# Optimization experiments

Measured on AMD Instinct MI355X. Metric: run time of the kernel, lower is better.

The kernel has to match this reference:

```python
import jax, jax.numpy as jnp
import numpy as np

N_USER = 50000
N_ITEM = 50000
E = 500000
D = 256
H = 8
DK = D // H
EPS = 1e-5
SQRT_DK = float(np.sqrt(DK))


def _layernorm(x, g, b):
    m = jnp.mean(x, axis=-1, keepdims=True)
    v = jnp.var(x, axis=-1, keepdims=True)
    return (x - m) * jax.lax.rsqrt(v + EPS) * g + b


def _etype_aggregate(h_src, h_dst, src, dst, n_dst, Wk, bk, Wq, bq, Wv, bv, pri, att, msg):
    # per-ntype K/Q/V projections, then per-relation head-wise transforms
    k = (h_src @ Wk + bk).reshape(-1, H, DK)
    v = (h_src @ Wv + bv).reshape(-1, H, DK)
    q = (h_dst @ Wq + bq).reshape(-1, H, DK)
    k = jnp.einsum('nhi,hij->nhj', k, att)
    v = jnp.einsum('nhi,hij->nhj', v, msg)
    # v_dot_u score per edge per head: [E, H]
    score = jnp.einsum('ehd,ehd->eh', q[dst], k[src]) * pri / SQRT_DK
    # edge_softmax normalized per destination node (per head)
    smax = jax.ops.segment_max(score, dst, num_segments=n_dst)
    ex = jnp.exp(score - smax[dst])
    ssum = jax.ops.segment_sum(ex, dst, num_segments=n_dst)
    a = ex / ssum[dst]
    # u_mul_e + sum reduce (zero-in-degree dst nodes get zeros, like DGL sum)
    t = jax.ops.segment_sum(v[src] * a[:, :, None], dst, num_segments=n_dst)
    return t.reshape(n_dst, D)


def _dst_update(t, h, Wa, ba, skip, g, b):
    alpha = jax.nn.sigmoid(skip)
    out = (t @ Wa + ba) * alpha + h * (1.0 - alpha)
    return _layernorm(out, g, b)


def _forward(h_user, h_item, src_ui, dst_ui, src_iu, dst_iu, Wk_user, bk_user, Wq_user, bq_user, Wv_user, bv_user, Wa_user, ba_user, ln_g_user, ln_b_user, skip_user, Wk_item, bk_item, Wq_item, bq_item, Wv_item, bv_item, Wa_item, ba_item, ln_g_item, ln_b_item, skip_item, pri_ui, att_ui, msg_ui, pri_iu, att_iu, msg_iu):
    # (user, click, item): k/v from src ntype 'user', q from dst ntype 'item'
    t_item = _etype_aggregate(h_user, h_item, src_ui, dst_ui, N_ITEM, Wk_user, bk_user, Wq_item, bq_item, Wv_user, bv_user, pri_ui, att_ui, msg_ui)
    # (item, rev_click, user)
    t_user = _etype_aggregate(h_item, h_user, src_iu, dst_iu, N_USER, Wk_item, bk_item, Wq_user, bq_user, Wv_item, bv_item, pri_iu, att_iu, msg_iu)
    # each ntype is dst of exactly one etype -> cross_reducer 'mean' is identity
    new_user = _dst_update(t_user, h_user, Wa_user, ba_user, skip_user, ln_g_user, ln_b_user)
    new_item = _dst_update(t_item, h_item, Wa_item, ba_item, skip_item, ln_g_item, ln_b_item)
    return jnp.stack([new_user, new_item])  # [2, N, D]


def setup_inputs() -> dict:
    key = jax.random.key(0)
    ks = jax.random.split(key, 16)

    def xavier(k, shape):
        s = np.sqrt(2.0 / (shape[-2] + shape[-1]))
        return (jax.random.normal(k, shape, dtype=jnp.float32) * s).astype(jnp.float32)

    inp = {}
    inp['h_user'] = jax.random.normal(ks[0], (N_USER, D), dtype=jnp.float32)
    inp['h_item'] = jax.random.normal(ks[1], (N_ITEM, D), dtype=jnp.float32)
    inp['src_ui'] = jax.random.randint(ks[2], (E,), 0, N_USER, dtype=jnp.int32)
    inp['dst_ui'] = jax.random.randint(ks[3], (E,), 0, N_ITEM, dtype=jnp.int32)
    inp['src_iu'] = jax.random.randint(ks[4], (E,), 0, N_ITEM, dtype=jnp.int32)
    inp['dst_iu'] = jax.random.randint(ks[5], (E,), 0, N_USER, dtype=jnp.int32)
    i = 6
    for nt in ['user', 'item']:
        for nm in ['k', 'q', 'v', 'a']:
            inp[f'W{nm}_{nt}'] = xavier(jax.random.fold_in(ks[i], hash(nm) % 1000), (D, D))
            inp[f'b{nm}_{nt}'] = jnp.zeros((D,), jnp.float32)
        i += 1
        inp[f'ln_g_{nt}'] = jnp.ones((D,), jnp.float32)
        inp[f'ln_b_{nt}'] = jnp.zeros((D,), jnp.float32)
        inp[f'skip_{nt}'] = jnp.ones((1,), jnp.float32)
    for et in ['ui', 'iu']:
        inp[f'pri_{et}'] = jnp.ones((H,), jnp.float32)
        inp[f'att_{et}'] = xavier(ks[i], (H, DK, DK)); i += 1
        inp[f'msg_{et}'] = xavier(ks[i], (H, DK, DK)); i += 1
    return inp


def reference(h_user, h_item, src_ui, dst_ui, src_iu, dst_iu, Wk_user, bk_user, Wq_user, bq_user, Wv_user, bv_user, Wa_user, ba_user, ln_g_user, ln_b_user, skip_user, Wk_item, bk_item, Wq_item, bq_item, Wv_item, bv_item, Wa_item, ba_item, ln_g_item, ln_b_item, skip_item, pri_ui, att_ui, msg_ui, pri_iu, att_iu, msg_iu):
    return _forward(h_user, h_item, src_ui, dst_ui, src_iu, dst_iu, Wk_user, bk_user, Wq_user, bq_user, Wv_user, bv_user, Wa_user, ba_user, ln_g_user, ln_b_user, skip_user, Wk_item, bk_item, Wq_item, bq_item, Wv_item, bv_item, Wa_item, ba_item, ln_g_item, ln_b_item, skip_item, pri_ui, att_ui, msg_ui, pri_iu, att_iu, msg_iu)
```

## Files before the change

### kernel.cpp

```cpp
#include <hip/hip_runtime.h>

#define NN 50000
#define DD 256
#define HH 8
#define EE 500000
#define INV_SQRT_DK 0.17677669529663687f

typedef __attribute__((ext_vector_type(8))) short bf16x8;
typedef __attribute__((ext_vector_type(4))) float f32x4;

__device__ __forceinline__ unsigned short f2bf(float f) {
    unsigned int u = __float_as_uint(f);
    u = (u + 0x7FFFu + ((u >> 16) & 1u)) >> 16;
    return (unsigned short)u;
}
__device__ __forceinline__ float bf2f(unsigned short u) {
    return __uint_as_float(((unsigned int)u) << 16);
}
__device__ __forceinline__ float bflo(unsigned int u) {
    return __uint_as_float(u << 16);
}
__device__ __forceinline__ float bfhi(unsigned int u) {
    return __uint_as_float(u & 0xFFFF0000u);
}

__global__ __launch_bounds__(256) void conv_bf16(const float* __restrict__ Xu,
                                                 const float* __restrict__ Xi,
                                                 unsigned short* __restrict__ Yu,
                                                 unsigned short* __restrict__ Yi) {
    const size_t ND = (size_t)NN * DD;
    size_t i = ((size_t)blockIdx.x * 256 + threadIdx.x) * 4;
    const float* X = Xu; unsigned short* Y = Yu;
    if (i >= ND) { X = Xi; Y = Yi; i -= ND; }
    float4 v = *(const float4*)&X[i];
    ushort4 o;
    o.x = f2bf(v.x); o.y = f2bf(v.y); o.z = f2bf(v.z); o.w = f2bf(v.w);
    *(ushort4*)&Y[i] = o;
}

__global__ __launch_bounds__(256) void fuse_kernel(const float* __restrict__ Wk_u, const float* __restrict__ bk_u,
                                                   const float* __restrict__ att_ui_,
                                                   const float* __restrict__ Wv_u, const float* __restrict__ bv_u,
                                                   const float* __restrict__ msg_ui_,
                                                   const float* __restrict__ Wk_i, const float* __restrict__ bk_i,
                                                   const float* __restrict__ att_iu_,
                                                   const float* __restrict__ Wv_i, const float* __restrict__ bv_i,
                                                   const float* __restrict__ msg_iu_,
                                                   unsigned short* __restrict__ BTu, float* __restrict__ beffU,
                                                   unsigned short* __restrict__ BTi, float* __restrict__ beffI) {
    int y = blockIdx.y;
    const float* W = (y == 0) ? Wk_u : (y == 1) ? Wv_u : (y == 2) ? Wk_i : Wv_i;
    const float* b = (y == 0) ? bk_u : (y == 1) ? bv_u : (y == 2) ? bk_i : bv_i;
    const float* T = (y == 0) ? att_ui_ : (y == 1) ? msg_ui_ : (y == 2) ? att_iu_ : msg_iu_;
    unsigned short* WT = ((y < 2) ? BTu : BTi) + ((y & 1) ? 256 * 256 : 0);
    float* be = ((y < 2) ? beffU : beffI) + ((y & 1) ? 256 : 0);
    int j = threadIdx.x;
    int h = j >> 5, jj = j & 31;
    const float* Th = T + h * 1024;
    if (blockIdx.x < 256) {
        int c = blockIdx.x;
        float acc = 0.f;
        #pragma unroll 8
        for (int i = 0; i < 32; ++i) acc += W[c * 256 + h * 32 + i] * Th[i * 32 + jj];
        WT[j * 256 + c] = f2bf(acc);
    } else {
        float acc = 0.f;
        #pragma unroll 8
        for (int i = 0; i < 32; ++i) acc += b[h * 32 + i] * Th[i * 32 + jj];
        be[j] = acc;
    }
}

__global__ __launch_bounds__(256) void convT_kernel(const float* __restrict__ Wq_u, const float* __restrict__ bq_u,
                                                    const float* __restrict__ Wq_i, const float* __restrict__ bq_i,
                                                    const float* __restrict__ Wa_u, const float* __restrict__ Wa_i,
                                                    unsigned short* __restrict__ BTu, float* __restrict__ beffU,
                                                    unsigned short* __restrict__ BTi, float* __restrict__ beffI,
                                                    unsigned short* __restrict__ WaTu, unsigned short* __restrict__ WaTi) {
    int y = blockIdx.y;
    const float* W = (y == 0) ? Wq_u : (y == 1) ? Wq_i : (y == 2) ? Wa_u : Wa_i;
    unsigned short* WT = (y == 0) ? BTu + 512 * 256 : (y == 1) ? BTi + 512 * 256 : (y == 2) ? WaTu : WaTi;
    int k = blockIdx.x, n = threadIdx.x;
    WT[n * 256 + k] = f2bf(W[k * 256 + n]);
    if (k == 0 && y < 2) {
        float* be = (y == 0) ? beffU : beffI;
        const float* bq = (y == 0) ? bq_u : bq_i;
        be[512 + n] = bq[n];
    }
}

__global__ void hist_kernel(const int* __restrict__ dst_ui, const int* __restrict__ dst_iu,
                            int* __restrict__ cnt) {
    int e = blockIdx.x * blockDim.x + threadIdx.x;
    if (e < EE) atomicAdd(&cnt[dst_ui[e]], 1);
    else if (e < 2 * EE) atomicAdd(&cnt[NN + dst_iu[e - EE]], 1);
}

__global__ __launch_bounds__(256) void alloc_kernel(const int* __restrict__ cnt,
                                                    int* __restrict__ start,
                                                    int* __restrict__ ctr) {
    int y = blockIdx.y;
    int i = blockIdx.x * 256 + threadIdx.x;
    int idx = y * NN + i;
    int v = (i < NN) ? cnt[idx] : 0;
    int lane = threadIdx.x & 63;
    int pre = v;
    #pragma unroll
    for (int o = 1; o < 64; o <<= 1) {
        int u = __shfl_up(pre, o, 64);
        if (lane >= o) pre += u;
    }
    int wsum = __shfl(pre, 63, 64);
    int base = 0;
    if (lane == 63) base = atomicAdd(&ctr[y], wsum);
    base = __shfl(base, 63, 64);
    if (i < NN) start[idx] = y * EE + base + pre - v;
}

__global__ void scatter_kernel(const int* __restrict__ dst_ui, const int* __restrict__ src_ui,
                               const int* __restrict__ dst_iu, const int* __restrict__ src_iu,
                               const int* __restrict__ start, int* __restrict__ cur,
                               int* __restrict__ srcid) {
    int e = blockIdx.x * blockDim.x + threadIdx.x;
    int d, s;
    if (e < EE) { d = dst_ui[e]; s = src_ui[e]; }
    else if (e < 2 * EE) { d = NN + dst_iu[e - EE]; s = src_iu[e - EE]; }
    else return;
    int pos = start[d] + atomicAdd(&cur[d], 1);
    srcid[pos] = s;
}

__global__ __launch_bounds__(256) void gemm_kvq(const unsigned short* __restrict__ Au,
                                                const unsigned short* __restrict__ Ai,
                                                const unsigned short* __restrict__ BTu,
                                                const unsigned short* __restrict__ BTi,
                                                const float* __restrict__ beffU,
                                                const float* __restrict__ beffI,
                                                unsigned short* __restrict__ KVu,
                                                unsigned short* __restrict__ KVi,
                                                unsigned short* __restrict__ Qu,
                                                unsigned short* __restrict__ Qi) {
    __shared__ bf16x8 As[128 * 5];
    __shared__ bf16x8 Bs[128 * 5];
    int z = blockIdx.z;
    const unsigned short* A = z ? Ai : Au;
    const unsigned short* BT = z ? BTi : BTu;
    const float* beff = z ? beffI : beffU;
    unsigned short* KV = z ? KVi : KVu;
    unsigned short* Qb = z ? Qi : Qu;
    int bm = blockIdx.x * 128, bn = blockIdx.y * 128;
    int tid = threadIdx.x;
    int lane = tid & 63, w = tid >> 6;
    int wm = (w & 1) * 64, wn = (w >> 1) * 64;
    int m16 = lane & 15, q = lane >> 4;
    f32x4 acc[4][4] = {};
    for (int k0 = 0; k0 < 256; k0 += 32) {
        #pragma unroll
        for (int cc = 0; cc < 2; ++cc) {
            int c = tid + cc * 256;
            int row = c >> 2, off8 = c & 3;
            int gr = bm + row;
            bf16x8 va = {};
            if (gr < NN) va = *(const bf16x8*)&A[(size_t)gr * 256 + k0 + off8 * 8];
            As[row * 5 + off8] = va;
            Bs[row * 5 + off8] = *(const bf16x8*)&BT[(size_t)(bn + row) * 256 + k0 + off8 * 8];
        }
        __syncthreads();
        bf16x8 af[4], bfr[4];
        #pragma unroll
        for (int i = 0; i < 4; ++i) af[i] = As[(wm + 16 * i + m16) * 5 + q];
        #pragma unroll
        for (int j = 0; j < 4; ++j) bfr[j] = Bs[(wn + 16 * j + m16) * 5 + q];
        #pragma unroll
        for (int i = 0; i < 4; ++i)
            #pragma unroll
            for (int j = 0; j < 4; ++j)
                acc[i][j] = __builtin_amdgcn_mfma_f32_16x16x32_bf16(af[i], bfr[j], acc[i][j], 0, 0, 0);
        __syncthreads();
    }
    #pragma unroll
    for (int i = 0; i < 4; ++i) {
        int rb = bm + wm + 16 * i + q * 4;
        #pragma unroll
        for (int j = 0; j < 4; ++j) {
            int col = bn + wn + 16 * j + m16;
            float bv = beff[col];
            #pragma unroll
            for (int r = 0; r < 4; ++r) {
                int row = rb + r;
                if (row < NN) {
                    unsigned short o = f2bf(acc[i][j][r] + bv);
                    if (bn < 512) {
                        int jc = col & 255;
                        int base = ((jc >> 2) << 3) + (jc & 3) + ((col & 256) ? 4 : 0);
                        KV[(size_t)row * 512 + base] = o;
                    } else {
                        Qb[(size_t)row * 256 + col - 512] = o;
                    }
                }
            }
        }
    }
}

__global__ __launch_bounds__(256) void gemm_out(const unsigned short* __restrict__ A0,
                                                const unsigned short* __restrict__ A1,
                                                const unsigned short* __restrict__ BT0,
                                                const unsigned short* __restrict__ BT1,
                                                const float* __restrict__ bias0,
                                                const float* __restrict__ bias1,
                                                float* __restrict__ C0,
                                                float* __restrict__ C1) {
    __shared__ bf16x8 As[128 * 5];
    __shared__ bf16x8 Bs[128 * 5];
    int z = blockIdx.z;
    const unsigned short* A = z ? A1 : A0;
    const unsigned short* BT = z ? BT1 : BT0;
    const float* bias = z ? bias1 : bias0;
    float* C = z ? C1 : C0;
    int bm = blockIdx.x * 128, bn = blockIdx.y * 128;
    int tid = threadIdx.x;
    int lane = tid & 63, w = tid >> 6;
    int wm = (w & 1) * 64, wn = (w >> 1) * 64;
    int m16 = lane & 15, q = lane >> 4;
    f32x4 acc[4][4] = {};
    for (int k0 = 0; k0 < 256; k0 += 32) {
        #pragma unroll
        for (int cc = 0; cc < 2; ++cc) {
            int c = tid + cc * 256;
            int row = c >> 2, off8 = c & 3;
            int gr = bm + row;
            bf16x8 va = {};
            if (gr < NN) va = *(const bf16x8*)&A[(size_t)gr * 256 + k0 + off8 * 8];
            As[row * 5 + off8] = va;
            Bs[row * 5 + off8] = *(const bf16x8*)&BT[(size_t)(bn + row) * 256 + k0 + off8 * 8];
        }
        __syncthreads();
        bf16x8 af[4], bfr[4];
        #pragma unroll
        for (int i = 0; i < 4; ++i) af[i] = As[(wm + 16 * i + m16) * 5 + q];
        #pragma unroll
        for (int j = 0; j < 4; ++j) bfr[j] = Bs[(wn + 16 * j + m16) * 5 + q];
        #pragma unroll
        for (int i = 0; i < 4; ++i)
            #pragma unroll
            for (int j = 0; j < 4; ++j)
                acc[i][j] = __builtin_amdgcn_mfma_f32_16x16x32_bf16(af[i], bfr[j], acc[i][j], 0, 0, 0);
        __syncthreads();
    }
    #pragma unroll
    for (int i = 0; i < 4; ++i) {
        int rb = bm + wm + 16 * i + q * 4;
        #pragma unroll
        for (int j = 0; j < 4; ++j) {
            int col = bn + wn + 16 * j + m16;
            float bv = bias[col];
            #pragma unroll
            for (int r = 0; r < 4; ++r) {
                int row = rb + r;
                if (row < NN) C[(size_t)row * 256 + col] = acc[i][j][r] + bv;
            }
        }
    }
}

__global__ __launch_bounds__(256) void fused_agg(const int* __restrict__ start,
                                                 const int* __restrict__ cnt,
                                                 const int* __restrict__ srcid,
                                                 const unsigned short* __restrict__ Qi,
                                                 const unsigned short* __restrict__ Qu,
                                                 const unsigned short* __restrict__ KVu,
                                                 const unsigned short* __restrict__ KVi,
                                                 const float* __restrict__ pri_ui,
                                                 const float* __restrict__ pri_iu,
                                                 unsigned short* __restrict__ tI16,
                                                 unsigned short* __restrict__ tU16) {
    int w = threadIdx.x >> 6;
    int lane = threadIdx.x & 63;
    int b = blockIdx.x * 4 + w;
    bool second = (b >= NN);
    int d = second ? b - NN : b;
    const unsigned short* Q = second ? Qu : Qi;
    const unsigned short* KV = second ? KVi : KVu;
    const float* pri = second ? pri_iu : pri_ui;
    unsigned short* T = second ? tU16 : tI16;

    int h = lane >> 3;
    float sscale = pri[h] * INV_SQRT_DK;
    ushort4 q4 = *(const ushort4*)&Q[(size_t)d * 256 + lane * 4];
    float qx = bf2f(q4.x), qy = bf2f(q4.y), qz = bf2f(q4.z), qw = bf2f(q4.w);

    int p0 = start[b], n = cnt[b];
    float a0 = 0.f, a1 = 0.f, a2 = 0.f, a3 = 0.f, l = 0.f;

    uint4 kv = {};
    if (n > 0) {
        int s = srcid[p0];
        kv = *(const uint4*)&KV[(size_t)s * 512 + lane * 8];
    }
    for (int p = 0; p < n; ++p) {
        uint4 cur = kv;
        if (p + 1 < n) {
            int s2 = srcid[p0 + p + 1];
            kv = *(const uint4*)&KV[(size_t)s2 * 512 + lane * 8];
        }
        float sc = qx * bflo(cur.x) + qy * bfhi(cur.x) + qz * bflo(cur.y) + qw * bfhi(cur.y);
        sc += __shfl_xor(sc, 1, 8);
        sc += __shfl_xor(sc, 2, 8);
        sc += __shfl_xor(sc, 4, 8);
        float wgt = __expf(sc * sscale);
        a0 += wgt * bflo(cur.z);
        a1 += wgt * bfhi(cur.z);
        a2 += wgt * bflo(cur.w);
        a3 += wgt * bfhi(cur.w);
        l += wgt;
    }
    float inv = (l > 0.f) ? 1.f / l : 0.f;
    ushort4 o;
    o.x = f2bf(a0 * inv); o.y = f2bf(a1 * inv);
    o.z = f2bf(a2 * inv); o.w = f2bf(a3 * inv);
    *(ushort4*)&T[(size_t)d * 256 + lane * 4] = o;
}

__global__ __launch_bounds__(256) void update_kernel(const float* __restrict__ tmpU,
                                                     const float* __restrict__ tmpI,
                                                     const float* __restrict__ hU,
                                                     const float* __restrict__ hI,
                                                     const float* __restrict__ skipU,
                                                     const float* __restrict__ skipI,
                                                     const float* __restrict__ gU, const float* __restrict__ bU,
                                                     const float* __restrict__ gI, const float* __restrict__ bI,
                                                     float* __restrict__ out) {
    int w = threadIdx.x >> 6;
    int lane = threadIdx.x & 63;
    int b = blockIdx.x * 4 + w;
    bool second = (b >= NN);
    int row = second ? b - NN : b;
    const float* tmp = second ? tmpI : tmpU;
    const float* hb = second ? hI : hU;
    const float* skp = second ? skipI : skipU;
    const float* g = second ? gI : gU;
    const float* bb = second ? bI : bU;
    float* o = out + (second ? (size_t)NN * DD : 0);

    float alpha = 1.f / (1.f + __expf(-skp[0]));
    float4 tm = *(const float4*)&tmp[(size_t)row * 256 + lane * 4];
    float4 hh = *(const float4*)&hb[(size_t)row * 256 + lane * 4];
    float x0 = tm.x * alpha + hh.x * (1.f - alpha);
    float x1 = tm.y * alpha + hh.y * (1.f - alpha);
    float x2 = tm.z * alpha + hh.z * (1.f - alpha);
    float x3 = tm.w * alpha + hh.w * (1.f - alpha);
    float s = x0 + x1 + x2 + x3;
    #pragma unroll
    for (int off = 32; off > 0; off >>= 1) s += __shfl_xor(s, off, 64);
    float mean = s * (1.f / 256.f);
    float d0 = x0 - mean, d1 = x1 - mean, d2 = x2 - mean, d3 = x3 - mean;
    float s2 = d0 * d0 + d1 * d1 + d2 * d2 + d3 * d3;
    #pragma unroll
    for (int off = 32; off > 0; off >>= 1) s2 += __shfl_xor(s2, off, 64);
    float rstd = rsqrtf(s2 * (1.f / 256.f) + 1e-5f);
    float4 g4 = *(const float4*)&g[lane * 4];
    float4 b4 = *(const float4*)&bb[lane * 4];
    float4 r;
    r.x = d0 * rstd * g4.x + b4.x;
    r.y = d1 * rstd * g4.y + b4.y;
    r.z = d2 * rstd * g4.z + b4.z;
    r.w = d3 * rstd * g4.w + b4.w;
    *(float4*)&o[(size_t)row * 256 + lane * 4] = r;
}

extern "C" void kernel_launch(void* const* d_in, const int* in_sizes, int n_in,
                              void* d_out, int out_size, void* d_ws, size_t ws_size,
                              hipStream_t stream) {
    const float* h_user  = (const float*)d_in[0];
    const float* h_item  = (const float*)d_in[1];
    const int*   src_ui  = (const int*)d_in[2];
    const int*   dst_ui  = (const int*)d_in[3];
    const int*   src_iu  = (const int*)d_in[4];
    const int*   dst_iu  = (const int*)d_in[5];
    const float* Wk_user = (const float*)d_in[6];
    const float* bk_user = (const float*)d_in[7];
    const float* Wq_user = (const float*)d_in[8];
    const float* bq_user = (const float*)d_in[9];
    const float* Wv_user = (const float*)d_in[10];
    const float* bv_user = (const float*)d_in[11];
    const float* Wa_user = (const float*)d_in[12];
    const float* ba_user = (const float*)d_in[13];
    const float* ln_g_user = (const float*)d_in[14];
    const float* ln_b_user = (const float*)d_in[15];
    const float* skip_user = (const float*)d_in[16];
    const float* Wk_item = (const float*)d_in[17];
    const float* bk_item = (const float*)d_in[18];
    const float* Wq_item = (const float*)d_in[19];
    const float* bq_item = (const float*)d_in[20];
    const float* Wv_item = (const float*)d_in[21];
    const float* bv_item = (const float*)d_in[22];
    const float* Wa_item = (const float*)d_in[23];
    const float* ba_item = (const float*)d_in[24];
    const float* ln_g_item = (const float*)d_in[25];
    const float* ln_b_item = (const float*)d_in[26];
    const float* skip_item = (const float*)d_in[27];
    const float* pri_ui = (const float*)d_in[28];
    const float* att_ui = (const float*)d_in[29];
    const float* msg_ui = (const float*)d_in[30];
    const float* pri_iu = (const float*)d_in[31];
    const float* att_iu = (const float*)d_in[32];
    const float* msg_iu = (const float*)d_in[33];
    float* out = (float*)d_out;

    const size_t ND = (size_t)NN * DD;

    unsigned short* up = (unsigned short*)d_ws;
    unsigned short* KVu = up;  up += (size_t)NN * 512;
    unsigned short* KVi = up;  up += (size_t)NN * 512;
    unsigned short* Qu  = up;  up += ND;
    unsigned short* Qi  = up;  up += ND;
    unsigned short* hU16 = up; up += ND;
    unsigned short* hI16 = up; up += ND;
    unsigned short* BTu = up;  up += 768 * 256;
    unsigned short* BTi = up;  up += 768 * 256;
    unsigned short* WaTu = up; up += 65536;
    unsigned short* WaTi = up; up += 65536;
    float* fp = (float*)up;
    float* beffU = fp; fp += 768;
    float* beffI = fp; fp += 768;
    int* ip = (int*)fp;
    int* cnt   = ip; ip += 2 * NN;
    int* cur   = ip; ip += 2 * NN;
    int* ctr   = ip; ip += 2;
    int* start = ip; ip += 2 * NN;
    int* srcid = ip; ip += 2 * EE;
    unsigned short* tU16 = hU16;
    unsigned short* tI16 = hI16;
    float* projU = (float*)KVu;
    float* projI = (float*)KVi;

    const int eb = (EE + 255) / 256;

    conv_bf16<<<2 * 12500, 256, 0, stream>>>(h_user, h_item, hU16, hI16);
    fuse_kernel<<<dim3(257, 4), 256, 0, stream>>>(Wk_user, bk_user, att_ui, Wv_user, bv_user, msg_ui,
                                                  Wk_item, bk_item, att_iu, Wv_item, bv_item, msg_iu,
                                                  BTu, beffU, BTi, beffI);
    convT_kernel<<<dim3(256, 4), 256, 0, stream>>>(Wq_user, bq_user, Wq_item, bq_item, Wa_user, Wa_item,
                                                   BTu, beffU, BTi, beffI, WaTu, WaTi);
    hipMemsetAsync(cnt, 0, (4 * NN + 2) * sizeof(int), stream);
    hist_kernel<<<2 * eb, 256, 0, stream>>>(dst_ui, dst_iu, cnt);
    alloc_kernel<<<dim3(196, 2), 256, 0, stream>>>(cnt, start, ctr);
    scatter_kernel<<<2 * eb, 256, 0, stream>>>(dst_ui, src_ui, dst_iu, src_iu, start, cur, srcid);

    gemm_kvq<<<dim3(391, 6, 2), 256, 0, stream>>>(hU16, hI16, BTu, BTi, beffU, beffI,
                                                  KVu, KVi, Qu, Qi);

    fused_agg<<<25000, 256, 0, stream>>>(start, cnt, srcid, Qi, Qu, KVu, KVi,
                                         pri_ui, pri_iu, tI16, tU16);

    gemm_out<<<dim3(391, 2, 2), 256, 0, stream>>>(tU16, tI16, WaTu, WaTi, ba_user, ba_item,
                                                  projU, projI);
    update_kernel<<<25000, 256, 0, stream>>>(projU, projI, h_user, h_item,
                                             skip_user, skip_item,
                                             ln_g_user, ln_b_user, ln_g_item, ln_b_item, out);
}
```

Measured before the change: 738.9 us.

## Pre-permute KV weight columns and stage GEMM epilogue through LDS for vector stores

The K/V fused weight columns are written in the interleaved KV layout during weight preparation, so the GEMM output columns already land in their final positions. The gemm_kvq epilogue then stages each 64-row half of the bf16 tile in shared memory and writes it out with 16-byte row-contiguous stores, replacing scattered 2-byte stores. This is meant to cut uncoalesced global write traffic in exchange for extra LDS traffic and two barriers per half.

Result: faster. 715.3 us (-3.2%).

```diff
diff --git a/kernel.cpp b/kernel.cpp
--- a/kernel.cpp
+++ b/kernel.cpp
@@ -52,22 +52,23 @@
     const float* W = (y == 0) ? Wk_u : (y == 1) ? Wv_u : (y == 2) ? Wk_i : Wv_i;
     const float* b = (y == 0) ? bk_u : (y == 1) ? bv_u : (y == 2) ? bk_i : bv_i;
     const float* T = (y == 0) ? att_ui_ : (y == 1) ? msg_ui_ : (y == 2) ? att_iu_ : msg_iu_;
-    unsigned short* WT = ((y < 2) ? BTu : BTi) + ((y & 1) ? 256 * 256 : 0);
-    float* be = ((y < 2) ? beffU : beffI) + ((y & 1) ? 256 : 0);
+    unsigned short* WT = (y < 2) ? BTu : BTi;
+    float* be = (y < 2) ? beffU : beffI;
     int j = threadIdx.x;
     int h = j >> 5, jj = j & 31;
+    int pj = ((j >> 2) << 3) + (j & 3) + ((y & 1) ? 4 : 0);
     const float* Th = T + h * 1024;
     if (blockIdx.x < 256) {
         int c = blockIdx.x;
         float acc = 0.f;
         #pragma unroll 8
         for (int i = 0; i < 32; ++i) acc += W[c * 256 + h * 32 + i] * Th[i * 32 + jj];
-        WT[j * 256 + c] = f2bf(acc);
+        WT[pj * 256 + c] = f2bf(acc);
     } else {
         float acc = 0.f;
         #pragma unroll 8
         for (int i = 0; i < 32; ++i) acc += b[h * 32 + i] * Th[i * 32 + jj];
-        be[j] = acc;
+        be[pj] = acc;
     }
 }
 
@@ -140,8 +141,9 @@
                                                 unsigned short* __restrict__ KVi,
                                                 unsigned short* __restrict__ Qu,
                                                 unsigned short* __restrict__ Qi) {
-    __shared__ bf16x8 As[128 * 5];
-    __shared__ bf16x8 Bs[128 * 5];
+    __shared__ __align__(16) char smem[20480];
+    bf16x8* As = (bf16x8*)smem;
+    bf16x8* Bs = (bf16x8*)(smem + 10240);
     int z = blockIdx.z;
     const unsigned short* A = z ? Ai : Au;
     const unsigned short* BT = z ? BTi : BTu;
@@ -178,28 +180,39 @@
                 acc[i][j] = __builtin_amdgcn_mfma_f32_16x16x32_bf16(af[i], bfr[j], acc[i][j], 0, 0, 0);
         __syncthreads();
     }
+    const bool isKV = (bn < 512);
+    unsigned short* dstb = isKV ? KV : Qb;
+    const int rowlen = isKV ? 512 : 256;
+    const int coloff = isKV ? bn : (bn - 512);
+    unsigned short* Cs = (unsigned short*)smem;
     #pragma unroll
-    for (int i = 0; i < 4; ++i) {
-        int rb = bm + wm + 16 * i + q * 4;
-        #pragma unroll
-        for (int j = 0; j < 4; ++j) {
-            int col = bn + wn + 16 * j + m16;
-            float bv = beff[col];
+    for (int half = 0; half < 2; ++half) {
+        if ((w & 1) == half) {
             #pragma unroll
-            for (int r = 0; r < 4; ++r) {
-                int row = rb + r;
-                if (row < NN) {
-                    unsigned short o = f2bf(acc[i][j][r] + bv);
-                    if (bn < 512) {
-                        int jc = col & 255;
-                        int base = ((jc >> 2) << 3) + (jc & 3) + ((col & 256) ? 4 : 0);
-                        KV[(size_t)row * 512 + base] = o;
-                    } else {
-                        Qb[(size_t)row * 256 + col - 512] = o;
-                    }
+            for (int i = 0; i < 4; ++i) {
+                int rloc = 16 * i + q * 4;
+                #pragma unroll
+                for (int j = 0; j < 4; ++j) {
+                    int cl = wn + 16 * j + m16;
+                    float bv = beff[bn + cl];
+                    #pragma unroll
+                    for (int r = 0; r < 4; ++r)
+                        Cs[(rloc + r) * 136 + cl] = f2bf(acc[i][j][r] + bv);
                 }
             }
         }
+        __syncthreads();
+        #pragma unroll
+        for (int it = 0; it < 4; ++it) {
+            int idx = it * 256 + tid;
+            int row = idx >> 4, seg = idx & 15;
+            int gr = bm + half * 64 + row;
+            if (gr < NN) {
+                bf16x8 v = *(const bf16x8*)&Cs[row * 136 + seg * 8];
+                *(bf16x8*)&dstb[(size_t)gr * rowlen + coloff + seg * 8] = v;
+            }
+        }
+        __syncthreads();
     }
 }
 
```
